# Kernel optimization log

Measured on AMD Instinct MI355X. Metric: run time of the kernel, lower is better.

The kernel has to match this reference:

```python
import jax, jax.numpy as jnp
import numpy as np

NODE_DIM = 128
NUM_IRREPS = 224          # 128 + 64 + 32 gates (one per irrep channel)
SPH_DIM = 480             # 128*1 + 64*3 + 32*5
HIDDEN = NODE_DIM + 2 * NUM_IRREPS  # 576
NUM_BASIS = 20
N_NODES = 10000
N_EDGES = 160000
# Each gate scalar is broadcast over its irrep's (2l+1) components.
_REPEATS = np.array([1] * 128 + [3] * 64 + [5] * 32)


def _expand_gate(g):
    # [E, 224] -> [E, 480], repeating each gate over its irrep dimension
    return jnp.repeat(g, _REPEATS, axis=-1, total_repeat_length=SPH_DIM)


def setup_inputs() -> dict:
    key = jax.random.key(0)
    ks = jax.random.split(key, 12)
    x_scalar = jax.random.normal(ks[0], (N_NODES, NODE_DIM), dtype=jnp.float32)
    x_spherical = jax.random.normal(ks[1], (N_NODES, SPH_DIM), dtype=jnp.float32)
    rbf = jax.random.uniform(ks[2], (N_EDGES, NUM_BASIS), dtype=jnp.float32)
    fcut = jax.random.uniform(ks[3], (N_EDGES, 1), dtype=jnp.float32)
    rsh = jax.random.normal(ks[4], (N_EDGES, SPH_DIM), dtype=jnp.float32)
    edge_index = jax.random.randint(ks[5], (2, N_EDGES), 0, N_NODES, dtype=jnp.int64)
    s1 = 1.0 / np.sqrt(NODE_DIM)
    s2 = 1.0 / np.sqrt(NUM_BASIS)
    W1 = jax.random.uniform(ks[6], (NODE_DIM, NODE_DIM), jnp.float32, -s1, s1)
    b1 = jnp.zeros((NODE_DIM,), jnp.float32)
    W2 = jax.random.uniform(ks[7], (NODE_DIM, HIDDEN), jnp.float32, -s1, s1)
    b2 = jnp.zeros((HIDDEN,), jnp.float32)
    Wr = jax.random.uniform(ks[8], (NUM_BASIS, HIDDEN), jnp.float32, -s2, s2)
    br = jnp.zeros((HIDDEN,), jnp.float32)
    return {"x_scalar": x_scalar, "x_spherical": x_spherical, "rbf": rbf,
            "fcut": fcut, "rsh": rsh, "edge_index": edge_index,
            "W1": W1, "b1": b1, "W2": W2, "b2": b2, "Wr": Wr, "br": br}


def reference(x_scalar, x_spherical, rbf, fcut, rsh, edge_index,
              W1, b1, W2, b2, Wr, br):
    src, dst = edge_index[0], edge_index[1]
    # scalar MLP: Linear -> SiLU -> Linear
    scalar_out = jax.nn.silu(x_scalar @ W1 + b1) @ W2 + b2          # [N, 576]
    filter_weight = (rbf @ Wr + br) * fcut                          # [E, 576]
    filter_out = scalar_out[dst] * filter_weight                    # [E, 576]
    gate_state = filter_out[:, :NUM_IRREPS]                         # [E, 224]
    gate_edge = filter_out[:, NUM_IRREPS:2 * NUM_IRREPS]            # [E, 224]
    message_scalar = filter_out[:, 2 * NUM_IRREPS:]                 # [E, 128]
    # ElementwiseTensorProduct(edge_irreps, '224x0e'): per-channel scalar gating
    message_spherical = (x_spherical[dst] * _expand_gate(gate_state)
                         + rsh * _expand_gate(gate_edge))           # [E, 480]
    new_scalar = x_scalar.at[src].add(message_scalar)
    new_spherical = x_spherical.at[src].add(message_spherical)
    return (new_scalar, new_spherical)
```

## Files before the change

### kernel.cpp

```cpp
#include <hip/hip_runtime.h>

#define NODE_DIM 128
#define NUM_IRREPS 224
#define SPH_DIM 480
#define HIDDEN 576
#define NUM_BASIS 20
#define N_NODES 10000
#define N_EDGES 160000
#define NPB 8
#define EB 16
#define NT 36
#define IRP 233
#define SCP 138

typedef __attribute__((ext_vector_type(8))) short short8v;
typedef __attribute__((ext_vector_type(4))) float f32x4;

__device__ __forceinline__ unsigned short f2bf(float f) {
    unsigned int u = __builtin_bit_cast(unsigned int, f);
    u = (u + 0x7fff + ((u >> 16) & 1)) >> 16;
    return (unsigned short)u;
}
__device__ __forceinline__ float bf2f(unsigned short h) {
    unsigned int u = ((unsigned int)h) << 16;
    return __builtin_bit_cast(float, u);
}

__global__ __launch_bounds__(256) void prep_kernel(
    const float* __restrict__ xs, const float* __restrict__ xsp,
    float* __restrict__ out,
    const int* __restrict__ eidx, int* __restrict__ counts,
    const float* __restrict__ Wr, unsigned short* __restrict__ bfrag,
    unsigned int* __restrict__ xpair) {
    const int stride = gridDim.x * blockDim.x;
    const int gt = blockIdx.x * blockDim.x + threadIdx.x;
    for (int i = gt; i < N_NODES * NODE_DIM; i += stride) out[i] = xs[i];
    float* o2 = out + (size_t)N_NODES * NODE_DIM;
    for (int i = gt; i < N_NODES * SPH_DIM; i += stride) o2[i] = xsp[i];
    for (int i = gt; i < N_NODES * 256; i += stride) {
        const int n = i >> 8, t = i & 255;
        const float* xr = xsp + (size_t)n * SPH_DIM;
        unsigned int lo = f2bf(xr[t]);
        unsigned int hi = (t < NUM_IRREPS) ? f2bf(xr[256 + t]) : 0u;
        xpair[i] = lo | (hi << 16);
    }
    if (gt < N_EDGES) atomicAdd(&counts[eidx[gt]], 1);
    if (blockIdx.x == gridDim.x - 1) {
        for (int idx = threadIdx.x; idx < NT * 64; idx += 256) {
            const int nt = idx >> 6, l = idx & 63;
            const int col = nt * 16 + (l & 15);
            const int kb = (l >> 4) * 8;
            #pragma unroll
            for (int j = 0; j < 8; ++j) {
                const int k = kb + j;
                bfrag[(size_t)idx * 8 + j] = (k < NUM_BASIS) ? f2bf(Wr[k * HIDDEN + col]) : (unsigned short)0;
            }
        }
    }
}

__global__ __launch_bounds__(128) void node_mlp(
    const float* __restrict__ x,
    const float* __restrict__ W1, const float* __restrict__ b1,
    const float* __restrict__ W2, const float* __restrict__ b2,
    unsigned short* __restrict__ so_bf) {
    __shared__ float xs[NPB][NODE_DIM];
    __shared__ float hs[NPB][NODE_DIM];
    const int tid = threadIdx.x;
    const int n0 = blockIdx.x * NPB;

    #pragma unroll
    for (int n = 0; n < NPB; ++n) {
        int node = n0 + n;
        xs[n][tid] = (node < N_NODES) ? x[(size_t)node * NODE_DIM + tid] : 0.f;
    }
    __syncthreads();

    float acc[NPB];
    #pragma unroll
    for (int n = 0; n < NPB; ++n) acc[n] = b1[tid];
    for (int k = 0; k < NODE_DIM; ++k) {
        float w = W1[k * NODE_DIM + tid];
        #pragma unroll
        for (int n = 0; n < NPB; ++n) acc[n] = fmaf(xs[n][k], w, acc[n]);
    }
    #pragma unroll
    for (int n = 0; n < NPB; ++n) {
        float v = acc[n];
        hs[n][tid] = v / (1.f + __expf(-v));
    }
    __syncthreads();

    for (int j = tid; j < HIDDEN; j += 128) {
        float a2[NPB];
        #pragma unroll
        for (int n = 0; n < NPB; ++n) a2[n] = b2[j];
        for (int k = 0; k < NODE_DIM; ++k) {
            float w = W2[k * HIDDEN + j];
            #pragma unroll
            for (int n = 0; n < NPB; ++n) a2[n] = fmaf(hs[n][k], w, a2[n]);
        }
        #pragma unroll
        for (int n = 0; n < NPB; ++n) {
            int node = n0 + n;
            if (node < N_NODES) so_bf[(size_t)node * HIDDEN + j] = f2bf(a2[n]);
        }
    }
}

__global__ __launch_bounds__(1024) void scan_kernel(const int* __restrict__ counts,
                                                    int* __restrict__ offsets,
                                                    int* __restrict__ cursor) {
    __shared__ int wsum[16];
    const int tid = threadIdx.x;
    int vals[10];
    int run = 0;
    #pragma unroll
    for (int i = 0; i < 10; ++i) {
        int idx = tid * 10 + i;
        int c = (idx < N_NODES) ? counts[idx] : 0;
        vals[i] = run;
        run += c;
    }
    const int lane = tid & 63, w = tid >> 6;
    int inc = run;
    #pragma unroll
    for (int off = 1; off < 64; off <<= 1) {
        int v = __shfl_up(inc, off);
        if (lane >= off) inc += v;
    }
    if (lane == 63) wsum[w] = inc;
    __syncthreads();
    if (w == 0) {
        int v = (lane < 16) ? wsum[lane] : 0;
        #pragma unroll
        for (int off = 1; off < 16; off <<= 1) {
            int u = __shfl_up(v, off);
            if (lane >= off) v += u;
        }
        if (lane < 16) wsum[lane] = v;
    }
    __syncthreads();
    const int wbase = (w > 0) ? wsum[w - 1] : 0;
    const int base = wbase + inc - run;
    #pragma unroll
    for (int i = 0; i < 10; ++i) {
        int idx = tid * 10 + i;
        if (idx < N_NODES) {
            int v = base + vals[i];
            offsets[idx] = v;
            cursor[idx] = v;
        }
    }
    if (tid == 1023) offsets[N_NODES] = wbase + inc;
}

__global__ __launch_bounds__(256) void scatter_kernel(const int* __restrict__ eidx,
                                                      int* __restrict__ cursor,
                                                      int* __restrict__ edge_order,
                                                      int* __restrict__ edge_src) {
    int i = blockIdx.x * blockDim.x + threadIdx.x;
    if (i < N_EDGES) {
        int s = eidx[i];
        int pos = atomicAdd(&cursor[s], 1);
        edge_order[pos] = i;
        edge_src[pos] = s;
    }
}

__global__ __launch_bounds__(256, 8) void edge_mfma(
    const unsigned int* __restrict__ xpair,
    const float* __restrict__ rbf, const float* __restrict__ fcut,
    const float* __restrict__ rsh, const int* __restrict__ eidx,
    const unsigned short* __restrict__ bfrag, const float* __restrict__ br,
    const unsigned short* __restrict__ so_bf,
    const int* __restrict__ edge_order, const int* __restrict__ edge_src,
    float* __restrict__ out_scalar, float* __restrict__ out_sph)
{
    __shared__ unsigned int   pair_s[EB][IRP];
    __shared__ unsigned short scal_s[EB][SCP];
    __shared__ int   e_s[EB];
    __shared__ int   src_s[EB];
    __shared__ int   dst_s[EB];
    __shared__ float fc_s[EB];

    const int t = threadIdx.x;
    const int base = blockIdx.x * EB;
    const int lane = t & 63, w = t >> 6;

    const int m_row = lane & 15;
    const int kb = (lane >> 4) * 8;
    const int e_row = edge_order[base + m_row];
    short8v a0;
    {
        const float* rrow = rbf + (size_t)e_row * NUM_BASIS;
        #pragma unroll
        for (int j = 0; j < 8; ++j) {
            const int k = kb + j;
            a0[j] = (k < NUM_BASIS) ? (short)f2bf(rrow[k]) : (short)0;
        }
    }

    if (t < EB) {
        int pos = base + t;
        int e = edge_order[pos];
        e_s[t]   = e;
        src_s[t] = edge_src[pos];
        dst_s[t] = eidx[N_EDGES + e];
        fc_s[t]  = fcut[e];
    }
    __syncthreads();

    {
        const int rbase = (lane >> 4) * 4;
        int   dA[4];
        float fA[4];
        #pragma unroll
        for (int r = 0; r < 4; ++r) { dA[r] = dst_s[rbase + r]; fA[r] = fc_s[rbase + r]; }
        #pragma unroll
        for (int i = 0; i < NT / 4; ++i) {
            const int nt = w * (NT / 4) + i;
            const short8v bf = *(const short8v*)(bfrag + (size_t)(nt * 64 + lane) * 8);
            f32x4 c0 = {0.f, 0.f, 0.f, 0.f};
            c0 = __builtin_amdgcn_mfma_f32_16x16x32_bf16(a0, bf, c0, 0, 0, 0);
            const int col = nt * 16 + (lane & 15);
            const float brc = br[col];
            #pragma unroll
            for (int r = 0; r < 4; ++r) {
                const int row = rbase + r;
                const float sov = bf2f(so_bf[(size_t)dA[r] * HIDDEN + col]);
                const float v = (c0[r] + brc) * fA[r] * sov;
                const unsigned short hv = f2bf(v);
                if (col < NUM_IRREPS) {
                    ((unsigned short*)&pair_s[row][col])[0] = hv;
                } else if (col < 2 * NUM_IRREPS) {
                    ((unsigned short*)&pair_s[row][col - NUM_IRREPS])[1] = hv;
                } else {
                    scal_s[row][col - 2 * NUM_IRREPS] = hv;
                }
            }
        }
    }
    __syncthreads();

    const int g1i = (t < 128) ? t : (128 + (t - 128) / 3);
    const int g2i = (t < 64) ? (128 + (128 + t) / 3) : (192 + (t - 64) / 5);

    float accS = 0.f, accD1 = 0.f, accD2 = 0.f;
    int cur_src = src_s[0];

    #pragma unroll 8
    for (int le = 0; le < EB; ++le) {
        const int s = src_s[le];
        if (s != cur_src) {
            atomicAdd(&out_sph[(size_t)cur_src * SPH_DIM + t], accD1);
            if (t < 224) atomicAdd(&out_sph[(size_t)cur_src * SPH_DIM + 256 + t], accD2);
            if (t < 128) atomicAdd(&out_scalar[(size_t)cur_src * NODE_DIM + t], accS);
            accD1 = accD2 = accS = 0.f;
            cur_src = s;
        }
        const int dst = dst_s[le];
        const int eg  = e_s[le];
        const unsigned int xp = xpair[(size_t)dst * 256 + t];
        const float rv1 = rsh[(size_t)eg * SPH_DIM + t];
        const unsigned int p1 = pair_s[le][g1i];
        accD1 = fmaf(bf2f((unsigned short)(xp & 0xffffu)), bf2f((unsigned short)(p1 & 0xffffu)),
                fmaf(rv1, bf2f((unsigned short)(p1 >> 16)), accD1));
        if (t < 224) {
            const float rv2 = rsh[(size_t)eg * SPH_DIM + 256 + t];
            const unsigned int p2 = pair_s[le][g2i];
            accD2 = fmaf(bf2f((unsigned short)(xp >> 16)), bf2f((unsigned short)(p2 & 0xffffu)),
                    fmaf(rv2, bf2f((unsigned short)(p2 >> 16)), accD2));
        }
        if (t < 128) accS += bf2f(scal_s[le][t]);
    }
    atomicAdd(&out_sph[(size_t)cur_src * SPH_DIM + t], accD1);
    if (t < 224) atomicAdd(&out_sph[(size_t)cur_src * SPH_DIM + 256 + t], accD2);
    if (t < 128) atomicAdd(&out_scalar[(size_t)cur_src * NODE_DIM + t], accS);
}

extern "C" void kernel_launch(void* const* d_in, const int* in_sizes, int n_in,
                              void* d_out, int out_size, void* d_ws, size_t ws_size,
                              hipStream_t stream) {
    const float* x_scalar    = (const float*)d_in[0];
    const float* x_spherical = (const float*)d_in[1];
    const float* rbf         = (const float*)d_in[2];
    const float* fcut        = (const float*)d_in[3];
    const float* rsh         = (const float*)d_in[4];
    const int*   eidx        = (const int*)d_in[5];
    const float* W1          = (const float*)d_in[6];
    const float* b1          = (const float*)d_in[7];
    const float* W2          = (const float*)d_in[8];
    const float* b2          = (const float*)d_in[9];
    const float* Wr          = (const float*)d_in[10];
    const float* br          = (const float*)d_in[11];

    float* out        = (float*)d_out;
    float* out_scalar = out;
    float* out_sph    = out + (size_t)N_NODES * NODE_DIM;

    unsigned short* so_bf   = (unsigned short*)d_ws;
    unsigned int*   xpair   = (unsigned int*)(so_bf + (size_t)N_NODES * HIDDEN);
    int*   counts     = (int*)(xpair + (size_t)N_NODES * 256);
    int*   offsets    = counts + N_NODES;
    int*   cursor     = offsets + N_NODES + 1;
    int*   edge_order = cursor + N_NODES;
    int*   edge_src   = edge_order + N_EDGES;
    unsigned short* bfrag = (unsigned short*)((((uintptr_t)(edge_src + N_EDGES)) + 15) & ~(uintptr_t)15);

    hipMemsetAsync(counts, 0, N_NODES * sizeof(int), stream);
    prep_kernel<<<2048, 256, 0, stream>>>(x_scalar, x_spherical, out, eidx, counts, Wr, bfrag, xpair);
    scan_kernel<<<1, 1024, 0, stream>>>(counts, offsets, cursor);
    scatter_kernel<<<(N_EDGES + 255) / 256, 256, 0, stream>>>(eidx, cursor, edge_order, edge_src);
    node_mlp<<<(N_NODES + NPB - 1) / NPB, 128, 0, stream>>>(x_scalar, W1, b1, W2, b2, so_bf);
    edge_mfma<<<N_EDGES / EB, 256, 0, stream>>>(xpair, rbf, fcut, rsh, eidx,
                                                bfrag, br, so_bf, edge_order, edge_src,
                                                out_scalar, out_sph);
}
```

Baseline: 356.3 us.

## Fuse node MLP into prep kernel, drop bf16 xpair, read fp32 spherical with prefetch

Merges the node MLP into the prep launch as extra blocks, so prep and MLP run concurrently in one launch and one launch is removed. It drops the bf16 packed copy of x_spherical and has the edge kernel read fp32 x_spherical directly, two components per thread, with software prefetch of the next edge's rows. It also changes the thread-to-element mapping and lowers the occupancy hint. The trade is fewer prep writes and conversions against more gather bandwidth in the edge kernel from fp32 reads.

```diff
diff --git a/kernel.cpp b/kernel.cpp
--- a/kernel.cpp
+++ b/kernel.cpp
@@ -7,11 +7,13 @@
 #define NUM_BASIS 20
 #define N_NODES 10000
 #define N_EDGES 160000
-#define NPB 8
+#define NPB 4
 #define EB 16
 #define NT 36
 #define IRP 233
 #define SCP 138
+#define PREP_BLOCKS 2048
+#define MLP_BLOCKS ((N_NODES + NPB - 1) / NPB)
 
 typedef __attribute__((ext_vector_type(8))) short short8v;
 typedef __attribute__((ext_vector_type(4))) float f32x4;
@@ -26,83 +28,76 @@
     return __builtin_bit_cast(float, u);
 }
 
-__global__ __launch_bounds__(256) void prep_kernel(
+__global__ __launch_bounds__(256) void prep_mlp_kernel(
     const float* __restrict__ xs, const float* __restrict__ xsp,
     float* __restrict__ out,
     const int* __restrict__ eidx, int* __restrict__ counts,
     const float* __restrict__ Wr, unsigned short* __restrict__ bfrag,
-    unsigned int* __restrict__ xpair) {
-    const int stride = gridDim.x * blockDim.x;
-    const int gt = blockIdx.x * blockDim.x + threadIdx.x;
-    for (int i = gt; i < N_NODES * NODE_DIM; i += stride) out[i] = xs[i];
-    float* o2 = out + (size_t)N_NODES * NODE_DIM;
-    for (int i = gt; i < N_NODES * SPH_DIM; i += stride) o2[i] = xsp[i];
-    for (int i = gt; i < N_NODES * 256; i += stride) {
-        const int n = i >> 8, t = i & 255;
-        const float* xr = xsp + (size_t)n * SPH_DIM;
-        unsigned int lo = f2bf(xr[t]);
-        unsigned int hi = (t < NUM_IRREPS) ? f2bf(xr[256 + t]) : 0u;
-        xpair[i] = lo | (hi << 16);
-    }
-    if (gt < N_EDGES) atomicAdd(&counts[eidx[gt]], 1);
-    if (blockIdx.x == gridDim.x - 1) {
-        for (int idx = threadIdx.x; idx < NT * 64; idx += 256) {
-            const int nt = idx >> 6, l = idx & 63;
-            const int col = nt * 16 + (l & 15);
-            const int kb = (l >> 4) * 8;
-            #pragma unroll
-            for (int j = 0; j < 8; ++j) {
-                const int k = kb + j;
-                bfrag[(size_t)idx * 8 + j] = (k < NUM_BASIS) ? f2bf(Wr[k * HIDDEN + col]) : (unsigned short)0;
-            }
-        }
-    }
-}
-
-__global__ __launch_bounds__(128) void node_mlp(
-    const float* __restrict__ x,
     const float* __restrict__ W1, const float* __restrict__ b1,
     const float* __restrict__ W2, const float* __restrict__ b2,
-    unsigned short* __restrict__ so_bf) {
-    __shared__ float xs[NPB][NODE_DIM];
-    __shared__ float hs[NPB][NODE_DIM];
-    const int tid = threadIdx.x;
-    const int n0 = blockIdx.x * NPB;
-
-    #pragma unroll
-    for (int n = 0; n < NPB; ++n) {
-        int node = n0 + n;
-        xs[n][tid] = (node < N_NODES) ? x[(size_t)node * NODE_DIM + tid] : 0.f;
-    }
-    __syncthreads();
-
-    float acc[NPB];
-    #pragma unroll
-    for (int n = 0; n < NPB; ++n) acc[n] = b1[tid];
+    unsigned short* __restrict__ so_bf)
+{
+    const int t = threadIdx.x;
+    if (blockIdx.x < PREP_BLOCKS) {
+        const int stride = PREP_BLOCKS * 256;
+        const int gt = blockIdx.x * 256 + t;
+        for (int i = gt; i < N_NODES * NODE_DIM; i += stride) out[i] = xs[i];
+        float* o2 = out + (size_t)N_NODES * NODE_DIM;
+        for (int i = gt; i < N_NODES * SPH_DIM; i += stride) o2[i] = xsp[i];
+        if (gt < N_EDGES) atomicAdd(&counts[eidx[gt]], 1);
+        if (blockIdx.x == PREP_BLOCKS - 1) {
+            for (int idx = t; idx < NT * 64; idx += 256) {
+                const int nt = idx >> 6, l = idx & 63;
+                const int col = nt * 16 + (l & 15);
+                const int kb = (l >> 4) * 8;
+                #pragma unroll
+                for (int j = 0; j < 8; ++j) {
+                    const int k = kb + j;
+                    bfrag[(size_t)idx * 8 + j] = (k < NUM_BASIS) ? f2bf(Wr[k * HIDDEN + col]) : (unsigned short)0;
+                }
+            }
+        }
+        return;
+    }
+    __shared__ float xsm[NPB][NODE_DIM];
+    __shared__ float hsm[NPB][NODE_DIM];
+    const int n0 = (blockIdx.x - PREP_BLOCKS) * NPB;
+    const int half = t >> 7;
+    const int tc = t & 127;
+
+    #pragma unroll
+    for (int i = 0; i < 2; ++i) {
+        const int nn = 2 * half + i;
+        const int node = n0 + nn;
+        xsm[nn][tc] = (node < N_NODES) ? xs[(size_t)node * NODE_DIM + tc] : 0.f;
+    }
+    __syncthreads();
+
+    float acc[2] = {b1[tc], b1[tc]};
     for (int k = 0; k < NODE_DIM; ++k) {
-        float w = W1[k * NODE_DIM + tid];
-        #pragma unroll
-        for (int n = 0; n < NPB; ++n) acc[n] = fmaf(xs[n][k], w, acc[n]);
-    }
-    #pragma unroll
-    for (int n = 0; n < NPB; ++n) {
-        float v = acc[n];
-        hs[n][tid] = v / (1.f + __expf(-v));
-    }
-    __syncthreads();
-
-    for (int j = tid; j < HIDDEN; j += 128) {
+        const float w = W1[k * NODE_DIM + tc];
+        #pragma unroll
+        for (int i = 0; i < 2; ++i) acc[i] = fmaf(xsm[2 * half + i][k], w, acc[i]);
+    }
+    #pragma unroll
+    for (int i = 0; i < 2; ++i) {
+        const float v = acc[i];
+        hsm[2 * half + i][tc] = v / (1.f + __expf(-v));
+    }
+    __syncthreads();
+
+    for (int j = t; j < HIDDEN; j += 256) {
         float a2[NPB];
         #pragma unroll
         for (int n = 0; n < NPB; ++n) a2[n] = b2[j];
         for (int k = 0; k < NODE_DIM; ++k) {
-            float w = W2[k * HIDDEN + j];
+            const float w = W2[k * HIDDEN + j];
             #pragma unroll
-            for (int n = 0; n < NPB; ++n) a2[n] = fmaf(hs[n][k], w, a2[n]);
+            for (int n = 0; n < NPB; ++n) a2[n] = fmaf(hsm[n][k], w, a2[n]);
         }
         #pragma unroll
         for (int n = 0; n < NPB; ++n) {
-            int node = n0 + n;
+            const int node = n0 + n;
             if (node < N_NODES) so_bf[(size_t)node * HIDDEN + j] = f2bf(a2[n]);
         }
     }
@@ -168,8 +163,12 @@
     }
 }
 
-__global__ __launch_bounds__(256, 8) void edge_mfma(
-    const unsigned int* __restrict__ xpair,
+__device__ __forceinline__ int gate_of(int d) {
+    return (d < 128) ? d : (d < 320) ? (128 + (d - 128) / 3) : (192 + (d - 320) / 5);
+}
+
+__global__ __launch_bounds__(256, 4) void edge_mfma(
+    const float* __restrict__ xsp,
     const float* __restrict__ rbf, const float* __restrict__ fcut,
     const float* __restrict__ rsh, const int* __restrict__ eidx,
     const unsigned short* __restrict__ bfrag, const float* __restrict__ br,
@@ -243,39 +242,54 @@
     }
     __syncthreads();
 
-    const int g1i = (t < 128) ? t : (128 + (t - 128) / 3);
-    const int g2i = (t < 64) ? (128 + (128 + t) / 3) : (192 + (t - 64) / 5);
-
-    float accS = 0.f, accD1 = 0.f, accD2 = 0.f;
+    const bool sphOn = (t < 240);
+    const int d0 = 2 * t;
+    const int g0 = sphOn ? gate_of(d0) : 0;
+    const int g1 = sphOn ? gate_of(d0 + 1) : 0;
+
+    float accS = 0.f, accD0 = 0.f, accD1 = 0.f;
     int cur_src = src_s[0];
 
-    #pragma unroll 8
+    float xq0, xq1, rq0, rq1;
+    if (sphOn) {
+        const float2 xv = *(const float2*)(xsp + (size_t)dst_s[0] * SPH_DIM + d0);
+        const float2 rv = *(const float2*)(rsh + (size_t)e_s[0]  * SPH_DIM + d0);
+        xq0 = xv.x; xq1 = xv.y; rq0 = rv.x; rq1 = rv.y;
+    }
+
+    #pragma unroll
     for (int le = 0; le < EB; ++le) {
+        float nx0, nx1, nr0, nr1;
+        if (sphOn && le + 1 < EB) {
+            const float2 xv = *(const float2*)(xsp + (size_t)dst_s[le + 1] * SPH_DIM + d0);
+            const float2 rv = *(const float2*)(rsh + (size_t)e_s[le + 1]  * SPH_DIM + d0);
+            nx0 = xv.x; nx1 = xv.y; nr0 = rv.x; nr1 = rv.y;
+        }
         const int s = src_s[le];
         if (s != cur_src) {
-            atomicAdd(&out_sph[(size_t)cur_src * SPH_DIM + t], accD1);
-            if (t < 224) atomicAdd(&out_sph[(size_t)cur_src * SPH_DIM + 256 + t], accD2);
+            if (sphOn) {
+                atomicAdd(&out_sph[(size_t)cur_src * SPH_DIM + d0],     accD0);
+                atomicAdd(&out_sph[(size_t)cur_src * SPH_DIM + d0 + 1], accD1);
+            }
             if (t < 128) atomicAdd(&out_scalar[(size_t)cur_src * NODE_DIM + t], accS);
-            accD1 = accD2 = accS = 0.f;
+            accD0 = accD1 = accS = 0.f;
             cur_src = s;
         }
-        const int dst = dst_s[le];
-        const int eg  = e_s[le];
-        const unsigned int xp = xpair[(size_t)dst * 256 + t];
-        const float rv1 = rsh[(size_t)eg * SPH_DIM + t];
-        const unsigned int p1 = pair_s[le][g1i];
-        accD1 = fmaf(bf2f((unsigned short)(xp & 0xffffu)), bf2f((unsigned short)(p1 & 0xffffu)),
-                fmaf(rv1, bf2f((unsigned short)(p1 >> 16)), accD1));
-        if (t < 224) {
-            const float rv2 = rsh[(size_t)eg * SPH_DIM + 256 + t];
-            const unsigned int p2 = pair_s[le][g2i];
-            accD2 = fmaf(bf2f((unsigned short)(xp >> 16)), bf2f((unsigned short)(p2 & 0xffffu)),
-                    fmaf(rv2, bf2f((unsigned short)(p2 >> 16)), accD2));
+        if (sphOn) {
+            const unsigned int p0 = pair_s[le][g0];
+            const unsigned int p1 = pair_s[le][g1];
+            accD0 = fmaf(xq0, bf2f((unsigned short)(p0 & 0xffffu)),
+                    fmaf(rq0, bf2f((unsigned short)(p0 >> 16)), accD0));
+            accD1 = fmaf(xq1, bf2f((unsigned short)(p1 & 0xffffu)),
+                    fmaf(rq1, bf2f((unsigned short)(p1 >> 16)), accD1));
         }
         if (t < 128) accS += bf2f(scal_s[le][t]);
-    }
-    atomicAdd(&out_sph[(size_t)cur_src * SPH_DIM + t], accD1);
-    if (t < 224) atomicAdd(&out_sph[(size_t)cur_src * SPH_DIM + 256 + t], accD2);
+        if (sphOn && le + 1 < EB) { xq0 = nx0; xq1 = nx1; rq0 = nr0; rq1 = nr1; }
+    }
+    if (sphOn) {
+        atomicAdd(&out_sph[(size_t)cur_src * SPH_DIM + d0],     accD0);
+        atomicAdd(&out_sph[(size_t)cur_src * SPH_DIM + d0 + 1], accD1);
+    }
     if (t < 128) atomicAdd(&out_scalar[(size_t)cur_src * NODE_DIM + t], accS);
 }
 
@@ -300,8 +314,7 @@
     float* out_sph    = out + (size_t)N_NODES * NODE_DIM;
 
     unsigned short* so_bf   = (unsigned short*)d_ws;
-    unsigned int*   xpair   = (unsigned int*)(so_bf + (size_t)N_NODES * HIDDEN);
-    int*   counts     = (int*)(xpair + (size_t)N_NODES * 256);
+    int*   counts     = (int*)(so_bf + (size_t)N_NODES * HIDDEN);
     int*   offsets    = counts + N_NODES;
     int*   cursor     = offsets + N_NODES + 1;
     int*   edge_order = cursor + N_NODES;
@@ -309,11 +322,12 @@
     unsigned short* bfrag = (unsigned short*)((((uintptr_t)(edge_src + N_EDGES)) + 15) & ~(uintptr_t)15);
 
     hipMemsetAsync(counts, 0, N_NODES * sizeof(int), stream);
-    prep_kernel<<<2048, 256, 0, stream>>>(x_scalar, x_spherical, out, eidx, counts, Wr, bfrag, xpair);
+    prep_mlp_kernel<<<PREP_BLOCKS + MLP_BLOCKS, 256, 0, stream>>>(
+        x_scalar, x_spherical, out, eidx, counts, Wr, bfrag,
+        W1, b1, W2, b2, so_bf);
     scan_kernel<<<1, 1024, 0, stream>>>(counts, offsets, cursor);
     scatter_kernel<<<(N_EDGES + 255) / 256, 256, 0, stream>>>(eidx, cursor, edge_order, edge_src);
-    node_mlp<<<(N_NODES + NPB - 1) / NPB, 128, 0, stream>>>(x_scalar, W1, b1, W2, b2, so_bf);
-    edge_mfma<<<N_EDGES / EB, 256, 0, stream>>>(xpair, rbf, fcut, rsh, eidx,
+    edge_mfma<<<N_EDGES / EB, 256, 0, stream>>>(x_spherical, rbf, fcut, rsh, eidx,
                                                 bfrag, br, so_bf, edge_order, edge_src,
                                                 out_scalar, out_sph);
 }
```

After: 285.1 us. 1.25x faster.
